# Optimization experiments

Hardware: AMD Instinct MI355X
Metric: run time of the kernel (lower is better)

## Reference

```python
import jax, jax.numpy as jnp
import numpy as np

# RoIAlign config (matches init_kwargs)
OUT_H = OUT_W = 7
SPATIAL_SCALE = 0.25
SAMPLING_RATIO = 2  # fixed grid per bin (aligned=True, detectron2-style)
N_IMG, C, H, W = 2, 256, 200, 304
N_ROIS = 512


def setup_inputs() -> dict:
    key = jax.random.key(0)
    kf, kb, kx1, ky1, kw, kh = jax.random.split(key, 6)
    features = jax.random.normal(kf, (N_IMG, C, H, W), dtype=jnp.float32)
    # rois: [R,5] = (batch_idx, x1, y1, x2, y2) in input-image coords (image ~ 1216x800)
    bidx = jax.random.randint(kb, (N_ROIS,), 0, N_IMG).astype(jnp.float32)
    x1 = jax.random.uniform(kx1, (N_ROIS,), minval=0.0, maxval=1100.0)
    y1 = jax.random.uniform(ky1, (N_ROIS,), minval=0.0, maxval=700.0)
    bw = jax.random.uniform(kw, (N_ROIS,), minval=8.0, maxval=116.0)
    bh = jax.random.uniform(kh, (N_ROIS,), minval=8.0, maxval=100.0)
    rois = jnp.stack([bidx, x1, y1, x1 + bw, y1 + bh], axis=1).astype(jnp.float32)
    return {"features": features, "rois": rois}


def roi_align(features, rois):
    N, C_, H_, W_ = features.shape
    G = SAMPLING_RATIO
    b = rois[:, 0].astype(jnp.int32)
    # aligned=True: scale then shift by -0.5 (continuous pixel model)
    x1 = rois[:, 1] * SPATIAL_SCALE - 0.5
    y1 = rois[:, 2] * SPATIAL_SCALE - 0.5
    x2 = rois[:, 3] * SPATIAL_SCALE - 0.5
    y2 = rois[:, 4] * SPATIAL_SCALE - 0.5
    roi_w = x2 - x1  # aligned: no clamp to min 1
    roi_h = y2 - y1
    bin_w = roi_w / OUT_W
    bin_h = roi_h / OUT_H

    # sample coordinates: per roi, OUT*G points along each axis
    iy = jnp.arange(OUT_H * G)
    ix = jnp.arange(OUT_W * G)
    # y = y1 + ph*bin_h + (s+0.5)*bin_h/G
    ys = y1[:, None] + (iy // G) * bin_h[:, None] + ((iy % G) + 0.5) * bin_h[:, None] / G  # [R, OUT_H*G]
    xs = x1[:, None] + (ix // G) * bin_w[:, None] + ((ix % G) + 0.5) * bin_w[:, None] / G  # [R, OUT_W*G]

    y = ys[:, :, None]  # [R, Py, 1]
    x = xs[:, None, :]  # [R, 1, Px]
    valid = ((y > -1.0) & (y < H_) & (x > -1.0) & (x < W_)).astype(features.dtype)  # [R,Py,Px]

    yc = jnp.clip(y, 0.0, H_ - 1)
    xc = jnp.clip(x, 0.0, W_ - 1)
    y0 = jnp.floor(yc).astype(jnp.int32)
    x0 = jnp.floor(xc).astype(jnp.int32)
    y1i = jnp.minimum(y0 + 1, H_ - 1)
    x1i = jnp.minimum(x0 + 1, W_ - 1)
    ly = yc - y0
    lx = xc - x0
    hy = 1.0 - ly
    hx = 1.0 - lx

    badv = b[:, None, None]
    Py, Px = OUT_H * G, OUT_W * G
    y0b = jnp.broadcast_to(y0, (rois.shape[0], Py, Px))
    y1b = jnp.broadcast_to(y1i, (rois.shape[0], Py, Px))
    x0b = jnp.broadcast_to(x0, (rois.shape[0], Py, Px))
    x1b = jnp.broadcast_to(x1i, (rois.shape[0], Py, Px))

    # advanced indexing: [R,Py,Px,C]
    v00 = features[badv, :, y0b, x0b]
    v01 = features[badv, :, y0b, x1b]
    v10 = features[badv, :, y1b, x0b]
    v11 = features[badv, :, y1b, x1b]

    w00 = (hy * hx) * valid
    w01 = (hy * lx) * valid
    w10 = (ly * hx) * valid
    w11 = (ly * lx) * valid

    samp = (w00[..., None] * v00 + w01[..., None] * v01 +
            w10[..., None] * v10 + w11[..., None] * v11)  # [R,Py,Px,C]
    # average pool over the GxG samples per bin
    R = rois.shape[0]
    out = samp.reshape(R, OUT_H, G, OUT_W, G, C_).mean(axis=(2, 4))  # [R,OUT_H,OUT_W,C]
    return jnp.transpose(out, (0, 3, 1, 2))  # [R,C,OUT_H,OUT_W]


def reference(features, rois):
    return roi_align(features, rois)
```

## Files before the change

kernel.cpp:

```cpp
#include <hip/hip_runtime.h>


#define OUT_H 7
#define OUT_W 7
constexpr float SPATIAL_SCALE = 0.25f;
constexpr int CN = 256;
constexpr int FH = 200;
constexpr int FW = 304;
constexpr int N_IMG = 2;
constexpr int N_ROIS = 512;
constexpr int PIX = FH * FW;
constexpr size_t PLANE = (size_t)PIX;
constexpr size_t NHWC_ELEMS = (size_t)N_IMG * PLANE * CN;
constexpr size_t NHWC_BF16_BYTES = NHWC_ELEMS * sizeof(unsigned short);

constexpr int CT = 64;
constexpr int PT = 128;

__device__ __forceinline__ unsigned short f2bf_rne(float f) {
    unsigned int u = __float_as_uint(f);
    unsigned int r = (u + 0x7FFFu + ((u >> 16) & 1u)) >> 16;
    return (unsigned short)r;
}

__global__ __launch_bounds__(256) void nchw_to_nhwc_bf16_tiled(
    const float* __restrict__ in, unsigned short* __restrict__ ws)
{
    const int pbase = blockIdx.x * PT;
    const int nc = blockIdx.y;
    const int n = nc >> 2;
    const int cbase = (nc & 3) * CT;

    __shared__ float tile[CT][PT + 1];

    {
        const int q = threadIdx.x & 31;
        const int r = threadIdx.x >> 5;
        const float* src = in + ((size_t)n * CN + cbase) * PLANE + pbase + 4 * q;
#pragma unroll
        for (int i = 0; i < 8; ++i) {
            const int c = r + 8 * i;
            const float4 v = *(const float4*)(src + (size_t)c * PLANE);
            tile[c][4 * q + 0] = v.x;
            tile[c][4 * q + 1] = v.y;
            tile[c][4 * q + 2] = v.z;
            tile[c][4 * q + 3] = v.w;
        }
    }
    __syncthreads();
    {
        const int cq = threadIdx.x & 7;
        const int p0 = threadIdx.x >> 3;
        unsigned short* dstbase =
            ws + ((size_t)n * PLANE + pbase) * CN + cbase + 8 * cq;
#pragma unroll
        for (int i2 = 0; i2 < 4; ++i2) {
            const int p = p0 + 32 * i2;
            uint4 pk;
            pk.x = (unsigned int)f2bf_rne(tile[8 * cq + 0][p]) |
                   ((unsigned int)f2bf_rne(tile[8 * cq + 1][p]) << 16);
            pk.y = (unsigned int)f2bf_rne(tile[8 * cq + 2][p]) |
                   ((unsigned int)f2bf_rne(tile[8 * cq + 3][p]) << 16);
            pk.z = (unsigned int)f2bf_rne(tile[8 * cq + 4][p]) |
                   ((unsigned int)f2bf_rne(tile[8 * cq + 5][p]) << 16);
            pk.w = (unsigned int)f2bf_rne(tile[8 * cq + 6][p]) |
                   ((unsigned int)f2bf_rne(tile[8 * cq + 7][p]) << 16);
            *(uint4*)(dstbase + (size_t)p * CN) = pk;
        }
    }
}

__global__ __launch_bounds__(128) void roi_align_nhwc_bf16(
    const unsigned short* __restrict__ ws,
    const float* __restrict__ rois,
    float* __restrict__ out)
{
    const int b = blockIdx.x;
    const int x = b & 7;
    const int s_id = b >> 3;
    const int r  = (s_id / 7) * 8 + x;
    const int ph = s_id % 7;
    const int t  = threadIdx.x;

    __shared__ float s_roi[5];
    __shared__ int   s_off[28][4];
    __shared__ float s_w[28][4];
    __shared__ int   s_b;

    if (t < 5) s_roi[t] = rois[r * 5 + t];
    __syncthreads();

    if (t < 28) {
        const int s  = t;
        const int gy = s / 14;
        const int ix = s % 14;
        const float x1 = s_roi[1] * SPATIAL_SCALE - 0.5f;
        const float y1 = s_roi[2] * SPATIAL_SCALE - 0.5f;
        const float x2 = s_roi[3] * SPATIAL_SCALE - 0.5f;
        const float y2 = s_roi[4] * SPATIAL_SCALE - 0.5f;
        const float bin_w = (x2 - x1) / OUT_W;
        const float bin_h = (y2 - y1) / OUT_H;
        const float y = y1 + ph * bin_h + (gy + 0.5f) * bin_h * 0.5f;
        const float xf = x1 + (ix >> 1) * bin_w + ((ix & 1) + 0.5f) * bin_w * 0.5f;
        const float validf =
            (y > -1.0f && y < (float)FH && xf > -1.0f && xf < (float)FW) ? 1.0f : 0.0f;
        const float yc = fminf(fmaxf(y, 0.0f), (float)(FH - 1));
        const float xc = fminf(fmaxf(xf, 0.0f), (float)(FW - 1));
        const int y0 = (int)floorf(yc);
        const int x0 = (int)floorf(xc);
        const int y1i = min(y0 + 1, FH - 1);
        const int x1i = min(x0 + 1, FW - 1);
        const float ly = yc - (float)y0;
        const float lx = xc - (float)x0;
        const float hy = 1.0f - ly;
        const float hx = 1.0f - lx;
        s_off[s][0] = ((y0  * FW + x0 ) * CN) * 2;
        s_off[s][1] = ((y0  * FW + x1i) * CN) * 2;
        s_off[s][2] = ((y1i * FW + x0 ) * CN) * 2;
        s_off[s][3] = ((y1i * FW + x1i) * CN) * 2;
        s_w[s][0] = hy * hx * validf;
        s_w[s][1] = hy * lx * validf;
        s_w[s][2] = ly * hx * validf;
        s_w[s][3] = ly * lx * validf;
    }
    if (t == 0) s_b = (int)s_roi[0];
    __syncthreads();

    const char* base =
        (const char*)(ws + (size_t)s_b * (PLANE * CN) + 2 * t);

    float acc0[OUT_W] = {0.f, 0.f, 0.f, 0.f, 0.f, 0.f, 0.f};
    float acc1[OUT_W] = {0.f, 0.f, 0.f, 0.f, 0.f, 0.f, 0.f};
#pragma unroll
    for (int s = 0; s < 28; ++s) {
        const int pw = (s % 14) >> 1;
#pragma unroll
        for (int k = 0; k < 4; ++k) {
            const unsigned int u = *(const unsigned int*)(base + s_off[s][k]);
            const float f0 = __uint_as_float(u << 16);
            const float f1 = __uint_as_float(u & 0xFFFF0000u);
            const float w = s_w[s][k];
            acc0[pw] = fmaf(w, f0, acc0[pw]);
            acc1[pw] = fmaf(w, f1, acc1[pw]);
        }
    }

    const size_t outbase = ((size_t)r * CN + 2 * t) * (OUT_H * OUT_W) + (size_t)ph * OUT_W;
#pragma unroll
    for (int pw = 0; pw < OUT_W; ++pw) {
        out[outbase + pw] = acc0[pw] * 0.25f;
        out[outbase + (OUT_H * OUT_W) + pw] = acc1[pw] * 0.25f;
    }
}

__global__ __launch_bounds__(256) void roi_align_nchw(
    const float* __restrict__ feat,
    const float* __restrict__ rois,
    float* __restrict__ out)
{
    const int r  = blockIdx.x;
    const int ph = blockIdx.y;
    const int c  = threadIdx.x;

    __shared__ float s_roi[5];
    __shared__ int   s_off[28][4];
    __shared__ float s_w[28][4];
    __shared__ int   s_b;

    if (threadIdx.x < 5) s_roi[threadIdx.x] = rois[r * 5 + threadIdx.x];
    __syncthreads();

    if (threadIdx.x < 28) {
        const int s  = threadIdx.x;
        const int gy = s / 14;
        const int ix = s % 14;
        const float x1 = s_roi[1] * SPATIAL_SCALE - 0.5f;
        const float y1 = s_roi[2] * SPATIAL_SCALE - 0.5f;
        const float x2 = s_roi[3] * SPATIAL_SCALE - 0.5f;
        const float y2 = s_roi[4] * SPATIAL_SCALE - 0.5f;
        const float bin_w = (x2 - x1) / OUT_W;
        const float bin_h = (y2 - y1) / OUT_H;
        const float y = y1 + ph * bin_h + (gy + 0.5f) * bin_h * 0.5f;
        const float xf = x1 + (ix >> 1) * bin_w + ((ix & 1) + 0.5f) * bin_w * 0.5f;
        const float validf =
            (y > -1.0f && y < (float)FH && xf > -1.0f && xf < (float)FW) ? 1.0f : 0.0f;
        const float yc = fminf(fmaxf(y, 0.0f), (float)(FH - 1));
        const float xc = fminf(fmaxf(xf, 0.0f), (float)(FW - 1));
        const int y0 = (int)floorf(yc);
        const int x0 = (int)floorf(xc);
        const int y1i = min(y0 + 1, FH - 1);
        const int x1i = min(x0 + 1, FW - 1);
        const float ly = yc - (float)y0;
        const float lx = xc - (float)x0;
        const float hy = 1.0f - ly;
        const float hx = 1.0f - lx;
        s_off[s][0] = y0  * FW + x0;
        s_off[s][1] = y0  * FW + x1i;
        s_off[s][2] = y1i * FW + x0;
        s_off[s][3] = y1i * FW + x1i;
        s_w[s][0] = hy * hx * validf;
        s_w[s][1] = hy * lx * validf;
        s_w[s][2] = ly * hx * validf;
        s_w[s][3] = ly * lx * validf;
    }
    if (threadIdx.x == 0) s_b = (int)s_roi[0];
    __syncthreads();

    const float* base = feat + ((size_t)s_b * CN + c) * PLANE;

    float acc[OUT_W] = {0.f, 0.f, 0.f, 0.f, 0.f, 0.f, 0.f};
#pragma unroll
    for (int s = 0; s < 28; ++s) {
        const float v0 = base[s_off[s][0]];
        const float v1 = base[s_off[s][1]];
        const float v2 = base[s_off[s][2]];
        const float v3 = base[s_off[s][3]];
        acc[(s % 14) >> 1] += s_w[s][0] * v0 + s_w[s][1] * v1 +
                              s_w[s][2] * v2 + s_w[s][3] * v3;
    }

    const size_t outbase = ((size_t)r * CN + c) * (OUT_H * OUT_W) + (size_t)ph * OUT_W;
#pragma unroll
    for (int pw = 0; pw < OUT_W; ++pw) {
        out[outbase + pw] = acc[pw] * 0.25f;
    }
}

extern "C" void kernel_launch(void* const* d_in, const int* in_sizes, int n_in,
                              void* d_out, int out_size, void* d_ws, size_t ws_size,
                              hipStream_t stream) {
    const float* feat = (const float*)d_in[0];
    const float* rois = (const float*)d_in[1];
    float* out = (float*)d_out;

    if (ws_size >= NHWC_BF16_BYTES) {
        unsigned short* ws = (unsigned short*)d_ws;
        dim3 tgrid(PIX / PT, (N_IMG * CN) / CT, 1);
        nchw_to_nhwc_bf16_tiled<<<tgrid, dim3(256, 1, 1), 0, stream>>>(feat, ws);
        roi_align_nhwc_bf16<<<dim3(N_ROIS * OUT_H, 1, 1), dim3(128, 1, 1), 0, stream>>>(
            ws, rois, out);
    } else {
        dim3 grid(N_ROIS, OUT_H, 1);
        roi_align_nchw<<<grid, dim3(256, 1, 1), 0, stream>>>(feat, rois, out);
    }
}
```

Before: 219.0 us.

## Factor bilinear weights separably and deduplicate shared sample rows/columns

```diff
diff --git a/kernel.cpp b/kernel.cpp
--- a/kernel.cpp
+++ b/kernel.cpp
@@ -83,65 +83,113 @@
     const int t  = threadIdx.x;
 
     __shared__ float s_roi[5];
-    __shared__ int   s_off[28][4];
-    __shared__ float s_w[28][4];
+    __shared__ int   s_ny;
+    __shared__ int   s_yoff[4];
+    __shared__ float s_wy[4];
+    __shared__ int   s_nx[OUT_W];
+    __shared__ int   s_xoff[OUT_W][4];
+    __shared__ float s_wx[OUT_W][4];
     __shared__ int   s_b;
 
     if (t < 5) s_roi[t] = rois[r * 5 + t];
     __syncthreads();
 
-    if (t < 28) {
-        const int s  = t;
-        const int gy = s / 14;
-        const int ix = s % 14;
+    if (t < 8) {
         const float x1 = s_roi[1] * SPATIAL_SCALE - 0.5f;
         const float y1 = s_roi[2] * SPATIAL_SCALE - 0.5f;
         const float x2 = s_roi[3] * SPATIAL_SCALE - 0.5f;
         const float y2 = s_roi[4] * SPATIAL_SCALE - 0.5f;
         const float bin_w = (x2 - x1) / OUT_W;
         const float bin_h = (y2 - y1) / OUT_H;
-        const float y = y1 + ph * bin_h + (gy + 0.5f) * bin_h * 0.5f;
-        const float xf = x1 + (ix >> 1) * bin_w + ((ix & 1) + 0.5f) * bin_w * 0.5f;
-        const float validf =
-            (y > -1.0f && y < (float)FH && xf > -1.0f && xf < (float)FW) ? 1.0f : 0.0f;
-        const float yc = fminf(fmaxf(y, 0.0f), (float)(FH - 1));
-        const float xc = fminf(fmaxf(xf, 0.0f), (float)(FW - 1));
-        const int y0 = (int)floorf(yc);
-        const int x0 = (int)floorf(xc);
-        const int y1i = min(y0 + 1, FH - 1);
-        const int x1i = min(x0 + 1, FW - 1);
-        const float ly = yc - (float)y0;
-        const float lx = xc - (float)x0;
-        const float hy = 1.0f - ly;
-        const float hx = 1.0f - lx;
-        s_off[s][0] = ((y0  * FW + x0 ) * CN) * 2;
-        s_off[s][1] = ((y0  * FW + x1i) * CN) * 2;
-        s_off[s][2] = ((y1i * FW + x0 ) * CN) * 2;
-        s_off[s][3] = ((y1i * FW + x1i) * CN) * 2;
-        s_w[s][0] = hy * hx * validf;
-        s_w[s][1] = hy * lx * validf;
-        s_w[s][2] = ly * hx * validf;
-        s_w[s][3] = ly * lx * validf;
-    }
-    if (t == 0) s_b = (int)s_roi[0];
-    __syncthreads();
-
-    const char* base =
-        (const char*)(ws + (size_t)s_b * (PLANE * CN) + 2 * t);
+        if (t == 0) {
+            int   col[4];
+            float w[4];
+#pragma unroll
+            for (int gy = 0; gy < 2; ++gy) {
+                const float y = y1 + ph * bin_h + (gy + 0.5f) * bin_h * 0.5f;
+                const float vy = (y > -1.0f && y < (float)FH) ? 1.0f : 0.0f;
+                const float yc = fminf(fmaxf(y, 0.0f), (float)(FH - 1));
+                const int y0 = (int)floorf(yc);
+                const int y1i = min(y0 + 1, FH - 1);
+                const float ly = yc - (float)y0;
+                col[2 * gy + 0] = y0;  w[2 * gy + 0] = (1.0f - ly) * vy;
+                col[2 * gy + 1] = y1i; w[2 * gy + 1] = ly * vy;
+            }
+            int   mcol[4];
+            float mw[4];
+            int n = 0;
+#pragma unroll
+            for (int k = 0; k < 4; ++k) {
+                if (w[k] == 0.0f) continue;
+                bool found = false;
+                for (int j = 0; j < n; ++j) {
+                    if (mcol[j] == col[k]) { mw[j] += w[k]; found = true; break; }
+                }
+                if (!found) { mcol[n] = col[k]; mw[n] = w[k]; ++n; }
+            }
+            for (int j = 0; j < n; ++j) {
+                s_yoff[j] = mcol[j] * (FW * CN * 2);
+                s_wy[j]   = mw[j];
+            }
+            s_ny = n;
+            s_b = (int)s_roi[0];
+        } else {
+            const int pw = t - 1;
+            int   col[4];
+            float w[4];
+#pragma unroll
+            for (int gx = 0; gx < 2; ++gx) {
+                const float xf = x1 + pw * bin_w + (gx + 0.5f) * bin_w * 0.5f;
+                const float vx = (xf > -1.0f && xf < (float)FW) ? 1.0f : 0.0f;
+                const float xc = fminf(fmaxf(xf, 0.0f), (float)(FW - 1));
+                const int x0 = (int)floorf(xc);
+                const int x1i = min(x0 + 1, FW - 1);
+                const float lx = xc - (float)x0;
+                col[2 * gx + 0] = x0;  w[2 * gx + 0] = (1.0f - lx) * vx;
+                col[2 * gx + 1] = x1i; w[2 * gx + 1] = lx * vx;
+            }
+            int   mcol[4];
+            float mw[4];
+            int n = 0;
+#pragma unroll
+            for (int k = 0; k < 4; ++k) {
+                if (w[k] == 0.0f) continue;
+                bool found = false;
+                for (int j = 0; j < n; ++j) {
+                    if (mcol[j] == col[k]) { mw[j] += w[k]; found = true; break; }
+                }
+                if (!found) { mcol[n] = col[k]; mw[n] = w[k]; ++n; }
+            }
+            for (int j = 0; j < n; ++j) {
+                s_xoff[pw][j] = mcol[j] * (CN * 2);
+                s_wx[pw][j]   = mw[j];
+            }
+            s_nx[pw] = n;
+        }
+    }
+    __syncthreads();
+
+    const char* base = (const char*)(ws + (size_t)s_b * (PLANE * CN)) + 4 * t;
 
     float acc0[OUT_W] = {0.f, 0.f, 0.f, 0.f, 0.f, 0.f, 0.f};
     float acc1[OUT_W] = {0.f, 0.f, 0.f, 0.f, 0.f, 0.f, 0.f};
-#pragma unroll
-    for (int s = 0; s < 28; ++s) {
-        const int pw = (s % 14) >> 1;
-#pragma unroll
-        for (int k = 0; k < 4; ++k) {
-            const unsigned int u = *(const unsigned int*)(base + s_off[s][k]);
-            const float f0 = __uint_as_float(u << 16);
-            const float f1 = __uint_as_float(u & 0xFFFF0000u);
-            const float w = s_w[s][k];
-            acc0[pw] = fmaf(w, f0, acc0[pw]);
-            acc1[pw] = fmaf(w, f1, acc1[pw]);
+
+    const int ny = s_ny;
+    for (int yi = 0; yi < ny; ++yi) {
+        const float wy = s_wy[yi];
+        const char* rb = base + s_yoff[yi];
+#pragma unroll
+        for (int pw = 0; pw < OUT_W; ++pw) {
+            float t0 = 0.f, t1 = 0.f;
+            const int nx = s_nx[pw];
+            for (int j = 0; j < nx; ++j) {
+                const unsigned int u = *(const unsigned int*)(rb + s_xoff[pw][j]);
+                const float wx = s_wx[pw][j];
+                t0 = fmaf(wx, __uint_as_float(u << 16), t0);
+                t1 = fmaf(wx, __uint_as_float(u & 0xFFFF0000u), t1);
+            }
+            acc0[pw] = fmaf(wy, t0, acc0[pw]);
+            acc1[pw] = fmaf(wy, t1, acc1[pw]);
         }
     }
 
```

Result: slower. 247.7 us (+13.1%).
